# Performance work log

Hardware: AMD Instinct MI355X
Metric: run time of the kernel (lower is better)

## Reference

```python
import jax, jax.numpy as jnp
import numpy as np

L_IN, L_K = 1, 1            # degree ranges (0..L)
C_IN, K_CH, H = 16, 8, 4    # in_channels, k_channels (per head), num_heads
C_OUT = H * K_CH            # 32
E, N_NODES, EMB = 32768, 4096, 64
M_IN, M_K = (L_IN + 1) ** 2, (L_K + 1) ** 2


def _so2_pairs(L_in, L_out):
    # enumerate SO(2)-equivariant weight blocks: for each order m, all (l_in, l_out)
    # pairs with l >= m; m=0 uses 1 matrix, m>0 uses 2 (real/imag parts).
    pairs, w = [], 0
    for m in range(min(L_in, L_out) + 1):
        for l_in in range(m, L_in + 1):
            for l_out in range(m, L_out + 1):
                pairs.append((m, l_in, l_out, w))
                w += 1 if m == 0 else 2
    return pairs, w

_PAIRS, NUM_W = _so2_pairs(L_IN, L_K)  # NUM_W = 6 for L_in=L_k=1


def so2_linear(x, W, L_in, L_out):
    # x: [E, (L_in+1)^2, Cin]; W: [NUM_W, Cin, Cout] (shared) or [E, NUM_W, Cin, Cout] (per-edge)
    per_edge = (W.ndim == 4)
    Cout = W.shape[-1]
    out = jnp.zeros((x.shape[0], (L_out + 1) ** 2, Cout), x.dtype)

    def mat(xs, w):
        return jnp.einsum('ec,eco->eo', xs, W[:, w]) if per_edge else xs @ W[w]

    pairs, _ = _so2_pairs(L_in, L_out)
    for m, l_in, l_out, w in pairs:
        i_in, i_out = l_in * (l_in + 1), l_out * (l_out + 1)  # flat index of (l, m=0)
        if m == 0:
            out = out.at[:, i_out].add(mat(x[:, i_in], w))
        else:
            xp, xn = x[:, i_in + m], x[:, i_in - m]
            out = out.at[:, i_out + m].add(mat(xp, w) - mat(xn, w + 1))
            out = out.at[:, i_out - m].add(mat(xp, w + 1) + mat(xn, w))
    return out


def segment_softmax(z, index, num_segments):
    # PyG-style softmax over ragged neighborhoods (max is detached, as in PyG)
    zmax = jax.lax.stop_gradient(jax.ops.segment_max(z, index, num_segments=num_segments))
    e = jnp.exp(z - zmax[index])
    denom = jax.ops.segment_sum(e, index, num_segments=num_segments)
    return e / denom[index]


def setup_inputs() -> dict:
    key = jax.random.key(0)
    ks = jax.random.split(key, 6)
    x_q = jax.random.normal(ks[0], (E, M_IN, C_IN), jnp.float32)
    x_k = jax.random.normal(ks[1], (E, M_IN, C_IN), jnp.float32)
    edge_emb = jax.random.normal(ks[2], (E, EMB), jnp.float32)
    index = jnp.sort(jax.random.randint(ks[3], (E,), 0, N_NODES))
    W_q = jax.random.normal(ks[4], (NUM_W, C_IN, C_OUT), jnp.float32) / np.sqrt(C_IN)
    W_p = jax.random.normal(ks[5], (EMB, NUM_W * C_IN * C_OUT), jnp.float32) / np.sqrt(EMB)
    return {"x_q": x_q, "x_k": x_k, "edge_emb": edge_emb, "index": index,
            "W_q": W_q, "W_p": W_p, "num_nodes": N_NODES}


def reference(x_q, x_k, edge_emb, index, W_q, W_p, num_nodes):
    # q_ij = W_Q x_i ; static SO2 weights
    q = so2_linear(x_q, W_q, L_IN, L_K).reshape(-1, M_K, H, K_CH)
    # k_ij = W_K(||r_ij||) x_j ; per-edge dynamic SO2 weights from edge embedding
    W_k = (edge_emb @ W_p).reshape(-1, NUM_W, C_IN, C_OUT)
    k = so2_linear(x_k, W_k, L_IN, L_K).reshape(-1, M_K, H, K_CH)
    scale = (K_CH // H) ** (-0.5)  # faithful to original: (k_channels // num_heads)**-0.5
    z = (q * k).sum((-1, -3)) * scale  # [E, H]
    return segment_softmax(z, index, num_nodes)
```

## Files before the change

### kernel.cpp

```cpp
#include <hip/hip_runtime.h>
#include <math.h>

#define E_TOTAL 32768
#define NUM_NODES 4096
#define SCALE 0.70710678118654752f

typedef __attribute__((ext_vector_type(8))) short bfrag;
typedef __attribute__((ext_vector_type(16))) float facc;

__device__ inline unsigned short f2bf(float f) {
  unsigned int u = __float_as_uint(f);
  unsigned int r = (u + 0x7FFFu + ((u >> 16) & 1u)) >> 16;
  return (unsigned short)r;
}
__device__ inline float bf2f(unsigned short s) {
  return __uint_as_float(((unsigned int)s) << 16);
}
__device__ inline void cvt8(const float* v, bfrag& hi, bfrag& lo) {
#pragma unroll
  for (int i = 0; i < 8; ++i) {
    unsigned short h = f2bf(v[i]);
    hi[i] = (short)h;
    lo[i] = (short)f2bf(v[i] - bf2f(h));
  }
}

__global__ __launch_bounds__(256) void prep_kernel(
    const float* __restrict__ Wp, const float* __restrict__ Wq,
    const int* __restrict__ index,
    unsigned short* __restrict__ fragWp, unsigned short* __restrict__ fragWq,
    int* __restrict__ offs)
{
  const int b = blockIdx.x, t = threadIdx.x;
  if (b < 96) {
    __shared__ unsigned short lds[4096];
    const int c = b / 6, w = b - c * 6;
    const int colbase = w * 512 + c * 32;
    const int cl = t & 31, dg = t >> 5;
#pragma unroll
    for (int i = 0; i < 8; ++i) {
      const int d = dg * 8 + i;
      const float v = Wp[(size_t)d * 3072 + colbase + cl];
      const unsigned short hi = f2bf(v);
      const unsigned short lo = f2bf(v - bf2f(hi));
      const int ks = d >> 4;
      const int lane = ((d >> 3) & 1) * 32 + cl;
      const int j = d & 7;
      lds[(ks * 2 + 0) * 512 + lane * 8 + j] = hi;
      lds[(ks * 2 + 1) * 512 + lane * 8 + j] = lo;
    }
    __syncthreads();
    unsigned short* dst = fragWp + (size_t)b * 4096;
    ((uint4*)dst)[t] = ((const uint4*)lds)[t];
    ((uint4*)dst)[t + 256] = ((const uint4*)lds)[t + 256];
  } else if (b < 103) {
    const int slot = b - 96;
    const int w = (slot == 6) ? 5 : slot;
    const float sgn = (slot == 6) ? -1.f : 1.f;
    for (int tt = t; tt < 512; tt += 256) {
      const int lane = tt >> 3, j = tt & 7;
      const int o = lane & 31, c = (lane >> 5) * 8 + j;
      const float v = sgn * Wq[(size_t)(w * 16 + c) * 32 + o];
      const unsigned short hi = f2bf(v);
      const unsigned short lo = f2bf(v - bf2f(hi));
      fragWq[slot * 1024 + lane * 8 + j] = hi;
      fragWq[slot * 1024 + 512 + lane * 8 + j] = lo;
    }
  } else {
    const int tg = (b - 103) * 256 + t;
    if (tg >= E_TOTAL) return;
    const int cur = index[tg];
    const int prev = (tg == 0) ? -1 : index[tg - 1];
    for (int n = prev + 1; n <= cur; ++n) offs[n] = tg;
    if (tg == E_TOTAL - 1)
      for (int n = cur + 1; n <= NUM_NODES; ++n) offs[n] = E_TOTAL;
  }
}

__global__ __launch_bounds__(256, 2) void main_kernel(
    const float* __restrict__ x_q, const float* __restrict__ x_k,
    const float* __restrict__ emb,
    const unsigned short* __restrict__ fragWp,
    const unsigned short* __restrict__ fragWq,
    float* __restrict__ z)
{
  __shared__ unsigned short fragbuf[2][8192];
  __shared__ float xk_t[64][65];
  __shared__ float zred[4][32][4];

  const int t = threadIdx.x;
  const int lane = t & 63, wv = t >> 6;
  const int pr = wv & 1, pg = wv >> 1;
  const int col = lane & 31, half = lane >> 5;
  const int eb = blockIdx.x * 64;
  const int el = pg * 32 + col;
  const int e = eb + el;

  {
    const int er = t >> 2, dq = (t & 3) * 16;
    const float* src = x_k + (size_t)(eb + er) * 64 + dq;
#pragma unroll
    for (int i = 0; i < 4; ++i) {
      float4 v = *(const float4*)(src + i * 4);
      xk_t[dq + i * 4 + 0][er] = v.x;
      xk_t[dq + i * 4 + 1][er] = v.y;
      xk_t[dq + i * 4 + 2][er] = v.z;
      xk_t[dq + i * 4 + 3][er] = v.w;
    }
  }

  bfrag ebh[4], ebl[4];
#pragma unroll
  for (int ks = 0; ks < 4; ++ks) {
    float tmp[8];
    *(float4*)&tmp[0] = *(const float4*)(emb + (size_t)e * 64 + ks * 16 + half * 8);
    *(float4*)&tmp[4] = *(const float4*)(emb + (size_t)e * 64 + ks * 16 + half * 8 + 4);
    cvt8(tmp, ebh[ks], ebl[ks]);
  }

  facc ka0 = {0}, ka1 = {0}, ka2 = {0}, ka3 = {0};

  {
    const unsigned short* gp = fragWp + wv * 2048 + lane * 8;
    unsigned short* lp = fragbuf[0] + wv * 2048;
#pragma unroll
    for (int i = 0; i < 4; ++i)
      __builtin_amdgcn_global_load_lds(
          (const __attribute__((address_space(1))) unsigned int*)(gp + i * 512),
          (__attribute__((address_space(3))) unsigned int*)(lp + i * 512), 16, 0, 0);
  }
  __syncthreads();

  float xkc0 = 0.f, xkc1 = 0.f, xkc2 = 0.f, xkc3 = 0.f;

  for (int c16 = 0; c16 < 16; ++c16) {
#pragma unroll
    for (int j = 0; j < 3; ++j) {
      const int it = c16 * 3 + j;
      const int p = it & 1;
      if (it < 47) {
        const unsigned short* gp =
            fragWp + (size_t)(it + 1) * 8192 + wv * 2048 + lane * 8;
        unsigned short* lp = fragbuf[p ^ 1] + wv * 2048;
#pragma unroll
        for (int i = 0; i < 4; ++i)
          __builtin_amdgcn_global_load_lds(
              (const __attribute__((address_space(1))) unsigned int*)(gp + i * 512),
              (__attribute__((address_space(3))) unsigned int*)(lp + i * 512), 16, 0, 0);
      }
      if (j == 0) {
        xkc0 = xk_t[c16][el];
        xkc1 = xk_t[16 + c16][el];
        xkc2 = xk_t[32 + c16][el];
        xkc3 = xk_t[48 + c16][el];
      }
      const unsigned short* fb = fragbuf[p] + pr * 4096;
      facc cc0 = {0.f}, cc1 = {0.f}, cc2 = {0.f};
#pragma unroll
      for (int ks = 0; ks < 4; ++ks) {
        bfrag wh = *(const bfrag*)(fb + (ks * 2 + 0) * 512 + lane * 8);
        bfrag wl = *(const bfrag*)(fb + (ks * 2 + 1) * 512 + lane * 8);
        cc0 = __builtin_amdgcn_mfma_f32_32x32x16_bf16(wh, ebh[ks], cc0, 0, 0, 0);
        cc1 = __builtin_amdgcn_mfma_f32_32x32x16_bf16(wh, ebl[ks], cc1, 0, 0, 0);
        cc2 = __builtin_amdgcn_mfma_f32_32x32x16_bf16(wl, ebh[ks], cc2, 0, 0, 0);
      }
      if (j < 2) {
        const float xv = (j == 0) ? xkc0 : xkc2;
        if (pr == 0) {
#pragma unroll
          for (int r = 0; r < 16; ++r)
            ka0[r] = fmaf(xv, cc0[r] + cc1[r] + cc2[r], ka0[r]);
        } else {
#pragma unroll
          for (int r = 0; r < 16; ++r)
            ka2[r] = fmaf(xv, cc0[r] + cc1[r] + cc2[r], ka2[r]);
        }
      } else {
        if (pr == 0) {
#pragma unroll
          for (int r = 0; r < 16; ++r) {
            const float s = cc0[r] + cc1[r] + cc2[r];
            ka1[r] = fmaf(xkc1, s, ka1[r]);
            ka3[r] = fmaf(xkc3, s, ka3[r]);
          }
        } else {
#pragma unroll
          for (int r = 0; r < 16; ++r) {
            const float s = cc0[r] + cc1[r] + cc2[r];
            ka1[r] = fmaf(xkc3, s, ka1[r]);
            ka3[r] = fmaf(-xkc1, s, ka3[r]);
          }
        }
      }
      __syncthreads();
    }
  }

  bfrag xqh[4], xql[4];
#pragma unroll
  for (int a = 0; a < 4; ++a) {
    float tmp[8];
    *(float4*)&tmp[0] = *(const float4*)(x_q + (size_t)e * 64 + a * 16 + half * 8);
    *(float4*)&tmp[4] = *(const float4*)(x_q + (size_t)e * 64 + a * 16 + half * 8 + 4);
    cvt8(tmp, xqh[a], xql[a]);
  }
  float zp0 = 0.f, zp1 = 0.f, zp2 = 0.f, zp3 = 0.f;
  const int QA1[4] = {0, 1, 0, 3}, QS1[4] = {0, 4, 1, 4};
  const int QA2[4] = {2, 3, 2, 1}, QS2[4] = {2, 5, 3, 6};
#pragma unroll
  for (int m = 0; m < 4; ++m) {
    facc qa = {0.f};
#pragma unroll
    for (int tm = 0; tm < 2; ++tm) {
      const int a = tm ? QA2[m] : QA1[m];
      const int sl = tm ? QS2[m] : QS1[m];
      bfrag wh, wl;
      *(uint4*)&wh = *(const uint4*)(fragWq + sl * 1024 + lane * 8);
      *(uint4*)&wl = *(const uint4*)(fragWq + sl * 1024 + 512 + lane * 8);
      qa = __builtin_amdgcn_mfma_f32_32x32x16_bf16(wh, xqh[a], qa, 0, 0, 0);
      qa = __builtin_amdgcn_mfma_f32_32x32x16_bf16(wh, xql[a], qa, 0, 0, 0);
      qa = __builtin_amdgcn_mfma_f32_32x32x16_bf16(wl, xqh[a], qa, 0, 0, 0);
    }
    const facc& km = (m == 0) ? ka0 : (m == 1) ? ka1 : (m == 2) ? ka2 : ka3;
#pragma unroll
    for (int r = 0; r < 16; ++r) {
      const float v = qa[r] * km[r];
      if (r < 4) zp0 += v;
      else if (r < 8) zp1 += v;
      else if (r < 12) zp2 += v;
      else zp3 += v;
    }
  }
  zp0 += __shfl_xor(zp0, 32);
  zp1 += __shfl_xor(zp1, 32);
  zp2 += __shfl_xor(zp2, 32);
  zp3 += __shfl_xor(zp3, 32);
  if (half == 0) {
    float4 v = {zp0, zp1, zp2, zp3};
    *(float4*)&zred[wv][col][0] = v;
  }
  __syncthreads();
  if (pr == 0 && half == 0) {
    float4 a = *(const float4*)&zred[wv][col][0];
    float4 b = *(const float4*)&zred[wv ^ 1][col][0];
    float4 o = {(a.x + b.x) * SCALE, (a.y + b.y) * SCALE,
                (a.z + b.z) * SCALE, (a.w + b.w) * SCALE};
    *(float4*)&z[(size_t)e * 4] = o;
  }
}

__global__ __launch_bounds__(256) void softmax_kernel(
    const float* __restrict__ z, const int* __restrict__ offs,
    float* __restrict__ out)
{
  const int node = blockIdx.x * 4 + (threadIdx.x >> 6);
  const int lane = threadIdx.x & 63;
  const int start = offs[node], end = offs[node + 1];
  if (start >= end) return;
  const int h = lane & 3, eo = lane >> 2;
  float m = -INFINITY;
  for (int e = start + eo; e < end; e += 16) m = fmaxf(m, z[(size_t)e * 4 + h]);
#pragma unroll
  for (int s = 4; s < 64; s <<= 1) m = fmaxf(m, __shfl_xor(m, s));
  float sum = 0.f;
  for (int e = start + eo; e < end; e += 16) sum += __expf(z[(size_t)e * 4 + h] - m);
#pragma unroll
  for (int s = 4; s < 64; s <<= 1) sum += __shfl_xor(sum, s);
  const float inv = 1.f / sum;
  for (int e = start + eo; e < end; e += 16)
    out[(size_t)e * 4 + h] = __expf(z[(size_t)e * 4 + h] - m) * inv;
}

extern "C" void kernel_launch(void* const* d_in, const int* in_sizes, int n_in,
                              void* d_out, int out_size, void* d_ws, size_t ws_size,
                              hipStream_t stream) {
  const float* x_q = (const float*)d_in[0];
  const float* x_k = (const float*)d_in[1];
  const float* emb = (const float*)d_in[2];
  const int* index = (const int*)d_in[3];
  const float* W_q = (const float*)d_in[4];
  const float* W_p = (const float*)d_in[5];
  float* out = (float*)d_out;

  char* ws = (char*)d_ws;
  float* z = (float*)ws;
  int* offs = (int*)(ws + 524288);
  unsigned short* fragWp = (unsigned short*)(ws + 524288 + 32768);
  unsigned short* fragWq = (unsigned short*)(ws + 524288 + 32768 + 786432);

  prep_kernel<<<231, 256, 0, stream>>>(W_p, W_q, index, fragWp, fragWq, offs);
  main_kernel<<<512, 256, 0, stream>>>(x_q, x_k, emb, fragWp, fragWq, z);
  softmax_kernel<<<1024, 256, 0, stream>>>(z, offs, out);
}
```

Before: 130.6 us.

## Load per-edge weight fragments directly into registers, dropping LDS staging and barriers

```diff
diff --git a/kernel.cpp b/kernel.cpp
--- a/kernel.cpp
+++ b/kernel.cpp
@@ -84,16 +84,15 @@
     const unsigned short* __restrict__ fragWq,
     float* __restrict__ z)
 {
-  __shared__ unsigned short fragbuf[2][8192];
   __shared__ float xk_t[64][65];
   __shared__ float zred[4][32][4];
 
   const int t = threadIdx.x;
   const int lane = t & 63, wv = t >> 6;
-  const int pr = wv & 1, pg = wv >> 1;
+  const int pr = wv & 1;
   const int col = lane & 31, half = lane >> 5;
   const int eb = blockIdx.x * 64;
-  const int el = pg * 32 + col;
+  const int el = (wv >> 1) * 32 + col;
   const int e = eb + el;
 
   {
@@ -120,80 +119,75 @@
 
   facc ka0 = {0}, ka1 = {0}, ka2 = {0}, ka3 = {0};
 
-  {
-    const unsigned short* gp = fragWp + wv * 2048 + lane * 8;
-    unsigned short* lp = fragbuf[0] + wv * 2048;
-#pragma unroll
-    for (int i = 0; i < 4; ++i)
-      __builtin_amdgcn_global_load_lds(
-          (const __attribute__((address_space(1))) unsigned int*)(gp + i * 512),
-          (__attribute__((address_space(3))) unsigned int*)(lp + i * 512), 16, 0, 0);
-  }
+  const unsigned short* fbase = fragWp + pr * 4096 + lane * 8;
+
+  bfrag curh[4], curl[4], nxth[4], nxtl[4];
+#pragma unroll
+  for (int ks = 0; ks < 4; ++ks) {
+    *(uint4*)&curh[ks] = *(const uint4*)(fbase + ks * 1024);
+    *(uint4*)&curl[ks] = *(const uint4*)(fbase + ks * 1024 + 512);
+  }
+
   __syncthreads();
 
   float xkc0 = 0.f, xkc1 = 0.f, xkc2 = 0.f, xkc3 = 0.f;
 
-  for (int c16 = 0; c16 < 16; ++c16) {
-#pragma unroll
-    for (int j = 0; j < 3; ++j) {
-      const int it = c16 * 3 + j;
-      const int p = it & 1;
-      if (it < 47) {
-        const unsigned short* gp =
-            fragWp + (size_t)(it + 1) * 8192 + wv * 2048 + lane * 8;
-        unsigned short* lp = fragbuf[p ^ 1] + wv * 2048;
-#pragma unroll
-        for (int i = 0; i < 4; ++i)
-          __builtin_amdgcn_global_load_lds(
-              (const __attribute__((address_space(1))) unsigned int*)(gp + i * 512),
-              (__attribute__((address_space(3))) unsigned int*)(lp + i * 512), 16, 0, 0);
+#pragma unroll 6
+  for (int it = 0; it < 48; ++it) {
+    const int j = it % 3;
+    {
+      const int itn = (it < 47) ? it + 1 : 47;
+      const unsigned short* gp = fbase + (size_t)itn * 8192;
+#pragma unroll
+      for (int ks = 0; ks < 4; ++ks) {
+        *(uint4*)&nxth[ks] = *(const uint4*)(gp + ks * 1024);
+        *(uint4*)&nxtl[ks] = *(const uint4*)(gp + ks * 1024 + 512);
       }
-      if (j == 0) {
-        xkc0 = xk_t[c16][el];
-        xkc1 = xk_t[16 + c16][el];
-        xkc2 = xk_t[32 + c16][el];
-        xkc3 = xk_t[48 + c16][el];
+    }
+    if (j == 0) {
+      const int c16 = it / 3;
+      xkc0 = xk_t[c16][el];
+      xkc1 = xk_t[16 + c16][el];
+      xkc2 = xk_t[32 + c16][el];
+      xkc3 = xk_t[48 + c16][el];
+    }
+    facc cc0 = {0.f}, cc1 = {0.f}, cc2 = {0.f};
+#pragma unroll
+    for (int ks = 0; ks < 4; ++ks) {
+      cc0 = __builtin_amdgcn_mfma_f32_32x32x16_bf16(curh[ks], ebh[ks], cc0, 0, 0, 0);
+      cc1 = __builtin_amdgcn_mfma_f32_32x32x16_bf16(curh[ks], ebl[ks], cc1, 0, 0, 0);
+      cc2 = __builtin_amdgcn_mfma_f32_32x32x16_bf16(curl[ks], ebh[ks], cc2, 0, 0, 0);
+    }
+    if (j < 2) {
+      const float xv = (j == 0) ? xkc0 : xkc2;
+      if (pr == 0) {
+#pragma unroll
+        for (int r = 0; r < 16; ++r)
+          ka0[r] = fmaf(xv, cc0[r] + cc1[r] + cc2[r], ka0[r]);
+      } else {
+#pragma unroll
+        for (int r = 0; r < 16; ++r)
+          ka2[r] = fmaf(xv, cc0[r] + cc1[r] + cc2[r], ka2[r]);
       }
-      const unsigned short* fb = fragbuf[p] + pr * 4096;
-      facc cc0 = {0.f}, cc1 = {0.f}, cc2 = {0.f};
-#pragma unroll
-      for (int ks = 0; ks < 4; ++ks) {
-        bfrag wh = *(const bfrag*)(fb + (ks * 2 + 0) * 512 + lane * 8);
-        bfrag wl = *(const bfrag*)(fb + (ks * 2 + 1) * 512 + lane * 8);
-        cc0 = __builtin_amdgcn_mfma_f32_32x32x16_bf16(wh, ebh[ks], cc0, 0, 0, 0);
-        cc1 = __builtin_amdgcn_mfma_f32_32x32x16_bf16(wh, ebl[ks], cc1, 0, 0, 0);
-        cc2 = __builtin_amdgcn_mfma_f32_32x32x16_bf16(wl, ebh[ks], cc2, 0, 0, 0);
-      }
-      if (j < 2) {
-        const float xv = (j == 0) ? xkc0 : xkc2;
-        if (pr == 0) {
-#pragma unroll
-          for (int r = 0; r < 16; ++r)
-            ka0[r] = fmaf(xv, cc0[r] + cc1[r] + cc2[r], ka0[r]);
-        } else {
-#pragma unroll
-          for (int r = 0; r < 16; ++r)
-            ka2[r] = fmaf(xv, cc0[r] + cc1[r] + cc2[r], ka2[r]);
+    } else {
+      if (pr == 0) {
+#pragma unroll
+        for (int r = 0; r < 16; ++r) {
+          const float s = cc0[r] + cc1[r] + cc2[r];
+          ka1[r] = fmaf(xkc1, s, ka1[r]);
+          ka3[r] = fmaf(xkc3, s, ka3[r]);
         }
       } else {
-        if (pr == 0) {
-#pragma unroll
-          for (int r = 0; r < 16; ++r) {
-            const float s = cc0[r] + cc1[r] + cc2[r];
-            ka1[r] = fmaf(xkc1, s, ka1[r]);
-            ka3[r] = fmaf(xkc3, s, ka3[r]);
-          }
-        } else {
-#pragma unroll
-          for (int r = 0; r < 16; ++r) {
-            const float s = cc0[r] + cc1[r] + cc2[r];
-            ka1[r] = fmaf(xkc3, s, ka1[r]);
-            ka3[r] = fmaf(-xkc1, s, ka3[r]);
-          }
+#pragma unroll
+        for (int r = 0; r < 16; ++r) {
+          const float s = cc0[r] + cc1[r] + cc2[r];
+          ka1[r] = fmaf(xkc3, s, ka1[r]);
+          ka3[r] = fmaf(-xkc1, s, ka3[r]);
         }
       }
-      __syncthreads();
-    }
+    }
+#pragma unroll
+    for (int ks = 0; ks < 4; ++ks) { curh[ks] = nxth[ks]; curl[ks] = nxtl[ks]; }
   }
 
   bfrag xqh[4], xql[4];
```

New measurement: 123.9 us. 5.1% less time.
